# Performance work log

Measured on AMD Instinct MI355X. Metric: run time of the kernel, lower is better.

The kernel has to match this reference:

```python
import jax, jax.numpy as jnp
import numpy as np

SIZE_MIN, SIZE_MAX = 10.0, 40.0
CROP = 28


def convert_to_box_list(x):
    # [B, C, W, H] -> [W*H, B, C]
    b, c, w, h = x.shape
    return jnp.transpose(x, (2, 3, 0, 1)).reshape(w * h, b, c)


def invert_convert_to_box_list(x, w, h):
    # [W*H, B, C] -> [B, C, W, H]
    n, b, c = x.shape
    return jnp.transpose(x.reshape(w, h, b, c), (2, 3, 0, 1))


def bilinear_sample(img, x, y):
    # img: [C, W, H]; x, y: pixel coords of shape S -> [C, *S]; zero outside.
    C, W, H = img.shape
    x0 = jnp.floor(x); y0 = jnp.floor(y)
    x1 = x0 + 1.0; y1 = y0 + 1.0
    wx1 = x - x0; wx0 = 1.0 - wx1
    wy1 = y - y0; wy0 = 1.0 - wy1
    def fetch(xi, yi):
        valid = ((xi >= 0) & (xi < W) & (yi >= 0) & (yi < H)).astype(img.dtype)
        xc = jnp.clip(xi, 0, W - 1).astype(jnp.int32)
        yc = jnp.clip(yi, 0, H - 1).astype(jnp.int32)
        return img[:, xc, yc] * valid
    return (fetch(x0, y0) * (wx0 * wy0) + fetch(x1, y0) * (wx1 * wy0)
            + fetch(x0, y1) * (wx0 * wy1) + fetch(x1, y1) * (wx1 * wy1))


def crop(bx, by, bw, bh, big, ws, hs):
    # bx..bh: [k, B]; big: [B, C, W, H] -> [k, B, C, ws, hs]
    u = (jnp.arange(ws) + 0.5) / ws
    v = (jnp.arange(hs) + 0.5) / hs
    xs = bx[..., None] - 0.5 * bw[..., None] + u * bw[..., None] - 0.5  # [k,B,ws]
    ys = by[..., None] - 0.5 * bh[..., None] + v * bh[..., None] - 0.5  # [k,B,hs]
    def one(xr, yr, img):
        X = jnp.broadcast_to(xr[:, None], (ws, hs))
        Y = jnp.broadcast_to(yr[None, :], (ws, hs))
        return bilinear_sample(img, X, Y)
    return jax.vmap(jax.vmap(one, (0, 0, 0)), (0, 0, None))(xs, ys, big)


def uncrop(bx, by, bw, bh, small, Wb, Hb):
    # small: [k, B, C, ws, hs] -> [k, B, C, Wb, Hb] (zero outside each box)
    ws, hs = small.shape[-2], small.shape[-1]
    Xc = jnp.arange(Wb) + 0.5
    Yc = jnp.arange(Hb) + 0.5
    xs = (Xc - (bx[..., None] - 0.5 * bw[..., None])) / bw[..., None] * ws - 0.5
    ys = (Yc - (by[..., None] - 0.5 * bh[..., None])) / bh[..., None] * hs - 0.5
    def one(xr, yr, img):
        X = jnp.broadcast_to(xr[:, None], (Wb, Hb))
        Y = jnp.broadcast_to(yr[None, :], (Wb, Hb))
        return bilinear_sample(img, X, Y)
    return jax.vmap(jax.vmap(one, (0, 0, 0)), (0, 0, 0))(xs, ys, small)


def tmaps_to_bb(tmaps, W_raw, H_raw):
    # tmaps: [B, 4, nw, nh] in (0,1) -> box lists [n_all, B]
    nw, nh = tmaps.shape[-2], tmaps.shape[-1]
    tx, ty, tw, th = tmaps[:, 0], tmaps[:, 1], tmaps[:, 2], tmaps[:, 3]
    ix = jnp.arange(nw, dtype=tmaps.dtype)[:, None]
    iy = jnp.arange(nh, dtype=tmaps.dtype)[None, :]
    bx_map = W_raw * (ix + tx) / nw
    by_map = H_raw * (iy + ty) / nh
    bw_map = SIZE_MIN + (SIZE_MAX - SIZE_MIN) * tw
    bh_map = SIZE_MIN + (SIZE_MAX - SIZE_MIN) * th
    tolist = lambda m: convert_to_box_list(m[:, None]).squeeze(-1)
    return tolist(bx_map), tolist(by_map), tolist(bw_map), tolist(bh_map)


def forward_core(logit_mu, zwhere_mu, zwhere_std, eps_zwhere, eps_zinstance,
                 features, w_zwhere, b_zwhere, w_enc, b_enc, w_dec, b_dec, n_objects_max):
    B, Cf, W_raw, H_raw = features.shape
    nw, nh = logit_mu.shape[-2], logit_mu.shape[-1]

    # zwhere posterior sample + KL vs N(0,1)
    zwhere_sample_map = zwhere_mu + zwhere_std * eps_zwhere
    zwhere_kl_map = 0.5 * (zwhere_mu ** 2 + zwhere_std ** 2) - jnp.log(zwhere_std) - 0.5

    # decode zwhere (1x1 conv) -> sigmoid tmaps -> boxes
    tmaps = jax.nn.sigmoid(jnp.einsum('bzwh,cz->bcwh', zwhere_sample_map, w_zwhere)
                           + b_zwhere[None, :, None, None])
    bx_all, by_all, bw_all, bh_all = tmaps_to_bb(tmaps, W_raw, H_raw)

    area_all = bw_all * bh_all
    area_map = invert_convert_to_box_list(area_all[..., None], nw, nh)

    # c sample = logit map (deterministic relaxation of the DPP/Bernoulli sample)
    c_sample_map = logit_mu
    prob_map = jax.nn.sigmoid(c_sample_map)
    c_all = convert_to_box_list(c_sample_map).squeeze(-1)   # [n_all, B]
    prob_all = convert_to_box_list(prob_map).squeeze(-1)

    # top-k per batch element (indices constant wrt grads)
    k = min(n_objects_max, c_all.shape[0])
    idx = jax.lax.stop_gradient(jax.lax.top_k(c_all.T, k)[1].T)  # [k, B]
    take = lambda t: jnp.take_along_axis(t, idx, axis=0)
    c_few, prob_few = take(c_all), take(prob_all)
    bx_few, by_few, bw_few, bh_few = take(bx_all), take(by_all), take(bw_all), take(bh_all)

    zwhere_sample_all = convert_to_box_list(zwhere_sample_map)  # [n_all, B, Z]
    zwhere_kl_all = convert_to_box_list(zwhere_kl_map)
    idx_z = idx[..., None]
    zwhere_sample_few = jnp.take_along_axis(zwhere_sample_all, idx_z, axis=0)
    zwhere_kl_few = jnp.take_along_axis(zwhere_kl_all, idx_z, axis=0)

    # crop full-res features at the k boxes -> [k, B, Cf, CROP, CROP]
    cropped = crop(bx_few, by_few, bw_few, bh_few, features, CROP, CROP)

    # encoder zinstance (flatten + linear -> mu, std)
    flat = cropped.reshape(k, B, -1)
    enc = jnp.einsum('kbf,df->kbd', flat, w_enc) + b_enc
    dim_z = enc.shape[-1] // 2
    zi_mu = enc[..., :dim_z]
    zi_std = jax.nn.softplus(enc[..., dim_z:]) + 1e-4
    zi_sample = zi_mu + zi_std * eps_zinstance
    zi_kl = 0.5 * (zi_mu ** 2 + zi_std ** 2) - jnp.log(zi_std) - 0.5

    # decoder zinstance (linear -> [k, B, 2, CROP, CROP])
    dec = jnp.einsum('kbz,fz->kbf', zi_sample, w_dec) + b_dec
    raw = dec.reshape(k, B, 2, CROP, CROP)
    small = jnp.concatenate([jax.nn.softplus(raw[..., :1, :, :]),
                             jax.nn.sigmoid(raw[..., 1:, :, :])], axis=-3)

    big_stuff = uncrop(bx_few, by_few, bw_few, bh_few,
                       small * c_few[..., None, None, None], W_raw, H_raw)
    big_weight = big_stuff[..., :1, :, :]
    big_img = big_stuff[..., 1:, :, :]

    # from_weights_to_masks over box dim (dim=-5 of [k,B,1,W,H])
    sum_w = jnp.sum(big_weight, axis=0, keepdims=True)
    big_mask = jnp.tanh(sum_w) * (big_weight / jnp.maximum(sum_w, 1e-6))
    big_mask_non = jnp.tanh(big_weight)

    return (prob_map, area_map, c_few, prob_few, bx_few, by_few, bw_few, bh_few,
            big_mask, big_mask_non, big_img,
            zwhere_sample_few, zwhere_kl_few, zi_sample, zi_kl)


def setup_inputs() -> dict:
    key = jax.random.key(0)
    ks = jax.random.split(key, 9)
    B, NW, NH = 8, 32, 32
    W_RAW = H_RAW = 128
    CF, ZW, ZI, K = 32, 8, 32, 48
    fan_in = CF * CROP * CROP
    return {
        "logit_mu": jax.random.normal(ks[0], (B, 1, NW, NH), jnp.float32),
        "zwhere_mu": 0.5 * jax.random.normal(ks[1], (B, ZW, NW, NH), jnp.float32),
        "zwhere_std": jax.random.uniform(ks[2], (B, ZW, NW, NH), jnp.float32, 0.1, 1.0),
        "eps_zwhere": jax.random.normal(ks[3], (B, ZW, NW, NH), jnp.float32),
        "eps_zinstance": jax.random.normal(ks[4], (K, B, ZI), jnp.float32),
        "features": jax.random.normal(ks[5], (B, CF, W_RAW, H_RAW), jnp.float32),
        "w_zwhere": 0.3 * jax.random.normal(ks[6], (4, ZW), jnp.float32),
        "b_zwhere": jnp.zeros((4,), jnp.float32),
        "w_enc": jax.random.normal(ks[7], (2 * ZI, fan_in), jnp.float32) / np.sqrt(fan_in).astype(np.float32),
        "b_enc": jnp.zeros((2 * ZI,), jnp.float32),
        "w_dec": jax.random.normal(ks[8], (2 * CROP * CROP, ZI), jnp.float32) / np.sqrt(ZI).astype(np.float32),
        "b_dec": jnp.zeros((2 * CROP * CROP,), jnp.float32),
        "n_objects_max": 48,
    }


def reference(logit_mu, zwhere_mu, zwhere_std, eps_zwhere, eps_zinstance, features,
              w_zwhere, b_zwhere, w_enc, b_enc, w_dec, b_dec, n_objects_max):
    return forward_core(logit_mu, zwhere_mu, zwhere_std, eps_zwhere, eps_zinstance,
                        features, w_zwhere, b_zwhere, w_enc, b_enc, w_dec, b_dec,
                        n_objects_max)
```

## Files before the change

kernel.cpp:

```cpp
#include <hip/hip_runtime.h>
#include <math.h>

#define B 8
#define NWD 32
#define NHD 32
#define NBOX 1024
#define ZWD 8
#define ZID 32
#define KOBJ 48
#define CFEAT 32
#define WRAW 128
#define HRAW 128
#define CR 28
#define CR2 784
#define FAN 25088
#define KB 384

#define OFF_PROB   0
#define OFF_AREA   8192
#define OFF_CFEW   16384
#define OFF_PFEW   16768
#define OFF_BXF    17152
#define OFF_BYF    17536
#define OFF_BWF    17920
#define OFF_BHF    18304
#define OFF_BMASK  18688
#define OFF_BMASKN 6310144
#define OFF_BIMG   12601600
#define OFF_ZWS    18893056
#define OFF_ZWK    18896128
#define OFF_ZIS    18899200
#define OFF_ZIK    18911488

#define WS_SMALL 32768

#define SCR_PART 0
#define SCR_WT   2752512

#define FSPLIT 112
#define FPB 224
#define MKB 16
#define KSTR 232
#define TAPN (MKB*28)

typedef __attribute__((ext_vector_type(8))) short bfrag;
typedef __attribute__((ext_vector_type(4))) float f32x4;

__device__ __forceinline__ float sigm(float x){ return 1.0f/(1.0f+expf(-x)); }
__device__ __forceinline__ float softpl(float x){ return fmaxf(x,0.0f) + log1pf(expf(-fabsf(x))); }
__device__ __forceinline__ float ftanh(float x){
  float t = __expf(2.0f*x);
  return 1.0f - __fdividef(2.0f, t + 1.0f);
}
__device__ __forceinline__ unsigned short f2bf(float f){
  unsigned u = __float_as_uint(f);
  unsigned r = u + 0x7FFFu + ((u >> 16) & 1u);
  return (unsigned short)(r >> 16);
}
__device__ __forceinline__ unsigned okey(float f){
  unsigned b = __float_as_uint(f);
  return b ^ ((b & 0x80000000u) ? 0xFFFFFFFFu : 0x80000000u);
}

__global__ __launch_bounds__(256) void wconv_kernel(
    const float* __restrict__ wenc, unsigned short* __restrict__ wt){
  const int gid = blockIdx.x*256 + threadIdx.x;
  const int lane = gid & 63;
  const int rest = gid >> 6;
  const int t = rest & 3;
  const int rest2 = rest >> 2;
  const int s = rest2 % 7;
  const int fs = rest2 / 7;
  const int d = t*16 + (lane & 15);
  const int k0 = fs*FPB + s*32 + (lane >> 4)*8;
  const float* src = wenc + (size_t)d*FAN + k0;
  float4 a = *(const float4*)src;
  float4 b = *(const float4*)(src + 4);
  unsigned long long p0 = (unsigned long long)f2bf(a.x)
    | ((unsigned long long)f2bf(a.y) << 16)
    | ((unsigned long long)f2bf(a.z) << 32)
    | ((unsigned long long)f2bf(a.w) << 48);
  unsigned long long p1 = (unsigned long long)f2bf(b.x)
    | ((unsigned long long)f2bf(b.y) << 16)
    | ((unsigned long long)f2bf(b.z) << 32)
    | ((unsigned long long)f2bf(b.w) << 48);
  unsigned short* dst = wt + (size_t)gid*8;
  *(unsigned long long*)dst       = p0;
  *(unsigned long long*)(dst + 4) = p1;
}

__global__ __launch_bounds__(256) void maps_topk_kernel(
    const float* __restrict__ logit, const float* __restrict__ zmu,
    const float* __restrict__ zstd, const float* __restrict__ zeps,
    const float* __restrict__ wz, const float* __restrict__ bz,
    float* __restrict__ out){
  const int b  = blockIdx.x >> 2;
  const int sb = blockIdx.x & 3;
  const int tid = threadIdx.x;
  __shared__ __align__(16) unsigned su[NBOX];
  #pragma unroll
  for (int u = 0; u < 4; u++){
    int j = tid + u*256;
    su[j] = okey(logit[b*NBOX + j]);
  }
  const int n = sb*256 + tid;
  const int w = n >> 5, h = n & 31;
  float acc0=bz[0], acc1=bz[1], acc2=bz[2], acc3=bz[3];
  #pragma unroll
  for(int z=0; z<ZWD; z++){
    int id = ((b*ZWD + z)*NWD + w)*NHD + h;
    float s = zmu[id] + zstd[id]*zeps[id];
    acc0 += s*wz[0*ZWD+z]; acc1 += s*wz[1*ZWD+z];
    acc2 += s*wz[2*ZWD+z]; acc3 += s*wz[3*ZWD+z];
  }
  float tx=sigm(acc0), ty=sigm(acc1), tw=sigm(acc2), th=sigm(acc3);
  float bx = (128.0f*((float)w + tx))/32.0f;
  float by = (128.0f*((float)h + ty))/32.0f;
  float bwv = 10.0f + 30.0f*tw;
  float bhv = 10.0f + 30.0f*th;
  float lg = logit[b*NBOX + n];
  out[OFF_PROB + b*NBOX + n] = sigm(lg);
  out[OFF_AREA + b*NBOX + n] = bwv*bhv;
  __syncthreads();
  const unsigned ui = su[n];
  const uint4* su4 = (const uint4*)su;
  int rank = 0;
  #pragma unroll 4
  for (int jq = 0; jq < NBOX/4; jq++){
    uint4 v = su4[jq];
    int j = jq*4;
    rank += (v.x > ui || (v.x == ui && j   < n)) ? 1 : 0;
    rank += (v.y > ui || (v.y == ui && j+1 < n)) ? 1 : 0;
    rank += (v.z > ui || (v.z == ui && j+2 < n)) ? 1 : 0;
    rank += (v.w > ui || (v.w == ui && j+3 < n)) ? 1 : 0;
  }
  if (rank < KOBJ){
    out[OFF_CFEW + rank*B + b] = lg;
    out[OFF_PFEW + rank*B + b] = sigm(lg);
    out[OFF_BXF  + rank*B + b] = bx;
    out[OFF_BYF  + rank*B + b] = by;
    out[OFF_BWF  + rank*B + b] = bwv;
    out[OFF_BHF  + rank*B + b] = bhv;
    #pragma unroll
    for(int z=0; z<ZWD; z++){
      int id = ((b*ZWD + z)*NWD + w)*NHD + h;
      float mu = zmu[id], sd = zstd[id];
      out[OFF_ZWS + (rank*B+b)*ZWD + z] = mu + sd*zeps[id];
      out[OFF_ZWK + (rank*B+b)*ZWD + z] = 0.5f*(mu*mu + sd*sd) - logf(sd) - 0.5f;
    }
  }
}

__global__ __launch_bounds__(256, 8) void enc_kernel(
    const float* __restrict__ feat, const unsigned short* __restrict__ wt,
    const float* __restrict__ outc, float* __restrict__ part){
  __shared__ __align__(16) unsigned short cl[MKB*KSTR];
  __shared__ float2 wxs[TAPN]; __shared__ int2 xos[TAPN];
  __shared__ float2 wys[TAPN]; __shared__ int2 yos[TAPN];
  __shared__ float rAx[MKB], rSx[MKB], rAy[MKB], rSy[MKB];
  const int tid = threadIdx.x;
  const int fs  = blockIdx.x % FSPLIT;
  const int kb0 = (blockIdx.x / FSPLIT) * MKB;
  if (tid < MKB){
    float bx = outc[OFF_BXF + kb0 + tid];
    float by = outc[OFF_BYF + kb0 + tid];
    float bw = outc[OFF_BWF + kb0 + tid];
    float bh = outc[OFF_BHF + kb0 + tid];
    float sx = bw * (1.0f/(float)CR), sy = bh * (1.0f/(float)CR);
    rSx[tid] = sx; rSy[tid] = sy;
    rAx[tid] = bx - 0.5f*bw + 0.5f*sx - 0.5f;
    rAy[tid] = by - 0.5f*bh + 0.5f*sy - 0.5f;
  }
  __syncthreads();
  #pragma unroll
  for (int it = 0; it < 4; it++){
    int idx = it*256 + tid;
    if (idx < 2*TAPN){
      int isy = idx >= TAPN;
      int q = idx - (isy ? TAPN : 0);
      int rr = q / 28, i = q - rr*28;
      float A = isy ? rAy[rr] : rAx[rr];
      float S = isy ? rSy[rr] : rSx[rr];
      float x = fmaf((float)i, S, A);
      float x0f = floorf(x); int x0 = (int)x0f;
      float w1 = x - x0f, w0 = 1.0f - w1;
      if ((unsigned)x0     >= WRAW) w0 = 0.f;
      if ((unsigned)(x0+1) >= WRAW) w1 = 0.f;
      int c0 = min(max(x0,0),WRAW-1), c1 = min(max(x0+1,0),WRAW-1);
      if (isy){ wys[q] = make_float2(w0,w1); yos[q] = make_int2(c0, c1); }
      else    { wxs[q] = make_float2(w0,w1); xos[q] = make_int2(c0*HRAW, c1*HRAW); }
    }
  }
  __syncthreads();
  const int fc0 = fs*FPB;
  #pragma unroll 2
  for (int u = 0; u < 14; u++){
    int idx = u*256 + tid;
    int rr = idx / FPB, ff = idx - rr*FPB;
    int f = fc0 + ff;
    int c = f / CR2; int p = f - c*CR2;
    int i = p / CR;  int j = p - i*CR;
    const float* img = feat + (size_t)(((kb0+rr) & (B-1))*CFEAT + c)*(WRAW*HRAW);
    float2 wx = wxs[rr*28 + i]; int2 xo = xos[rr*28 + i];
    float2 wy = wys[rr*28 + j]; int2 yo = yos[rr*28 + j];
    float v = (img[xo.x+yo.x]*wy.x + img[xo.x+yo.y]*wy.y)*wx.x
            + (img[xo.y+yo.x]*wy.x + img[xo.y+yo.y]*wy.y)*wx.y;
    cl[rr*KSTR + ff] = f2bf(v);
  }
  __syncthreads();
  const int lane = tid & 63, wv = tid >> 6;
  const int lr = lane & 15, lg = lane >> 4;
  f32x4 acc = {0.f,0.f,0.f,0.f};
  const unsigned short* arow  = &cl[lr*KSTR + lg*8];
  const unsigned short* bbase = wt + (size_t)fs*14336 + wv*512 + lane*8;
  #pragma unroll
  for (int s = 0; s < 7; s++){
    bfrag a = *(const bfrag*)(arow + s*32);
    bfrag b = *(const bfrag*)(bbase + s*2048);
    acc = __builtin_amdgcn_mfma_f32_16x16x32_bf16(a, b, acc, 0, 0, 0);
  }
  float* dst = part + ((size_t)fs*KB + kb0)*64;
  #pragma unroll
  for (int r = 0; r < 4; r++){
    int row = lg*4 + r;
    dst[row*64 + wv*16 + lr] = acc[r];
  }
}

__global__ __launch_bounds__(256) void zi_dec_kernel(
    const float* __restrict__ part, const float* __restrict__ benc,
    const float* __restrict__ ieps, const float* __restrict__ wdec,
    const float* __restrict__ bdec, float* __restrict__ out,
    float* __restrict__ ws){
  int kb = blockIdx.x;
  int d = threadIdx.x & 63, seg = threadIdx.x >> 6;
  float s0=0.f, s1=0.f, s2=0.f, s3=0.f;
  for (int f = seg; f < FSPLIT; f += 16){
    s0 += part[((size_t)(f   )*KB + kb)*64 + d];
    s1 += part[((size_t)(f+ 4)*KB + kb)*64 + d];
    s2 += part[((size_t)(f+ 8)*KB + kb)*64 + d];
    s3 += part[((size_t)(f+12)*KB + kb)*64 + d];
  }
  __shared__ float red[4][64];
  __shared__ float zs[ZID];
  __shared__ float cf_s;
  red[seg][d] = (s0+s1) + (s2+s3);
  __syncthreads();
  if (threadIdx.x < ZID){
    int dd = threadIdx.x;
    float mu = benc[dd]     + red[0][dd]     + red[1][dd]     + red[2][dd]     + red[3][dd];
    float pe = benc[ZID+dd] + red[0][ZID+dd] + red[1][ZID+dd] + red[2][ZID+dd] + red[3][ZID+dd];
    float sd = softpl(pe) + 1e-4f;
    float zsv = mu + sd*ieps[kb*ZID + dd];
    out[OFF_ZIS + kb*ZID + dd] = zsv;
    out[OFF_ZIK + kb*ZID + dd] = 0.5f*(mu*mu + sd*sd) - logf(sd) - 0.5f;
    zs[dd] = zsv;
  }
  if (threadIdx.x == 0) cf_s = out[OFF_CFEW + kb];
  __syncthreads();
  float cf = cf_s;
  for (int f = threadIdx.x; f < 2*CR2; f += 256){
    float a = bdec[f];
    #pragma unroll
    for (int q = 0; q < 8; q++){
      float4 w4 = *(const float4*)&wdec[f*ZID + q*4];
      a = fmaf(zs[q*4+0], w4.x, a);
      a = fmaf(zs[q*4+1], w4.y, a);
      a = fmaf(zs[q*4+2], w4.z, a);
      a = fmaf(zs[q*4+3], w4.w, a);
    }
    float v = (f < CR2) ? softpl(a) : sigm(a);
    ws[WS_SMALL + (size_t)kb*(2*CR2) + f] = v*cf;
  }
}

__global__ __launch_bounds__(256) void uncrop_compose_kernel(
    const float* __restrict__ ws, float* __restrict__ out){
  const int t = blockIdx.x*256 + threadIdx.x;
  const int b = t >> 14, p = t & 16383;
  const int X = p >> 7, Y = p & 127;
  __shared__ float sAx[KOBJ], sSx[KOBJ], sAy[KOBJ], sSy[KOBJ];
  if (threadIdx.x < KOBJ){
    int k = threadIdx.x;
    float bx = out[OFF_BXF + k*B + b], bw = out[OFF_BWF + k*B + b];
    float by = out[OFF_BYF + k*B + b], bh = out[OFF_BHF + k*B + b];
    float ix = __fdividef((float)CR, bw), iy = __fdividef((float)CR, bh);
    sSx[k] = ix; sAx[k] = (0.5f*bw - bx)*ix - 0.5f;
    sSy[k] = iy; sAy[k] = (0.5f*bh - by)*iy - 0.5f;
  }
  __syncthreads();
  const float xc = (float)X + 0.5f, yc = (float)Y + 0.5f;
  float wr[KOBJ];
  float sum = 0.f;
  #pragma unroll
  for (int k = 0; k < KOBJ; k++){
    float x = fmaf(xc, sSx[k], sAx[k]);
    float y = fmaf(yc, sSy[k], sAy[k]);
    const float* sm = ws + WS_SMALL + (size_t)(k*B + b)*(2*CR2);
    float x0f = floorf(x), y0f = floorf(y);
    int x0 = (int)x0f, y0 = (int)y0f;
    float wx1 = x - x0f, wx0 = 1.0f - wx1;
    float wy1 = y - y0f, wy0 = 1.0f - wy1;
    if ((unsigned)x0     >= CR) wx0 = 0.f;
    if ((unsigned)(x0+1) >= CR) wx1 = 0.f;
    if ((unsigned)y0     >= CR) wy0 = 0.f;
    if ((unsigned)(y0+1) >= CR) wy1 = 0.f;
    int x0c = min(max(x0,0),CR-1), x1c = min(max(x0+1,0),CR-1);
    int y0c = min(max(y0,0),CR-1), y1c = min(max(y0+1,0),CR-1);
    const float* r0 = sm + x0c*CR;
    const float* r1 = sm + x1c*CR;
    float v0 = (r0[y0c]*wy0 + r0[y1c]*wy1)*wx0 + (r1[y0c]*wy0 + r1[y1c]*wy1)*wx1;
    const float* q0 = r0 + CR2;
    const float* q1 = r1 + CR2;
    float v1 = (q0[y0c]*wy0 + q0[y1c]*wy1)*wx0 + (q1[y0c]*wy0 + q1[y1c]*wy1)*wx1;
    wr[k] = v0; sum += v0;
    out[OFF_BIMG + (size_t)(k*B + b)*16384 + p] = v1;
  }
  float th = ftanh(sum);
  float inv = 1.0f / fmaxf(sum, 1e-6f);
  #pragma unroll
  for (int k = 0; k < KOBJ; k++){
    size_t o = (size_t)(k*B + b)*16384 + p;
    out[OFF_BMASK  + o] = th * (wr[k] * inv);
    out[OFF_BMASKN + o] = ftanh(wr[k]);
  }
}

extern "C" void kernel_launch(void* const* d_in, const int* in_sizes, int n_in,
                              void* d_out, int out_size, void* d_ws, size_t ws_size,
                              hipStream_t stream) {
  (void)in_sizes; (void)n_in; (void)out_size; (void)ws_size;
  const float* logit = (const float*)d_in[0];
  const float* zmu   = (const float*)d_in[1];
  const float* zstd  = (const float*)d_in[2];
  const float* zeps  = (const float*)d_in[3];
  const float* ieps  = (const float*)d_in[4];
  const float* feat  = (const float*)d_in[5];
  const float* wz    = (const float*)d_in[6];
  const float* bz    = (const float*)d_in[7];
  const float* wenc  = (const float*)d_in[8];
  const float* benc  = (const float*)d_in[9];
  const float* wdec  = (const float*)d_in[10];
  const float* bdec  = (const float*)d_in[11];
  float* out = (float*)d_out;
  float* ws  = (float*)d_ws;
  float* scr = out + OFF_BMASK;
  float* part = scr + SCR_PART;
  unsigned short* wt = (unsigned short*)(scr + SCR_WT);

  wconv_kernel        <<<(FAN*64)/(256*8), 256, 0, stream>>>(wenc, wt);
  maps_topk_kernel    <<<B*4, 256, 0, stream>>>(logit, zmu, zstd, zeps, wz, bz, out);
  enc_kernel          <<<(KB/MKB)*FSPLIT, 256, 0, stream>>>(feat, wt, out, part);
  zi_dec_kernel       <<<KB, 256, 0, stream>>>(part, benc, ieps, wdec, bdec, out, ws);
  uncrop_compose_kernel<<<(B*WRAW*HRAW)/256, 256, 0, stream>>>(ws, out);
}
```

Measured before the change: 95.50 us.

## Fuse prep kernels and double-buffer encoder sampling across feature chunks

Merges the weight-conversion and top-k map kernels into one launch. The encoder kernel now handles four feature chunks per block, cutting the split factor from 112 to 28, and double-buffers the sampled crop tile in shared memory so bilinear gathers for the next chunk overlap the MFMA on the current one. Fewer partial sums leave a smaller reduction in zi_dec. The trade-off is fewer encoder blocks, which lowers parallelism, and more shared memory per block, which may reduce occupancy.

```diff
diff --git a/kernel.cpp b/kernel.cpp
--- a/kernel.cpp
+++ b/kernel.cpp
@@ -37,8 +37,10 @@
 #define SCR_PART 0
 #define SCR_WT   2752512
 
-#define FSPLIT 112
-#define FPB 224
+#define FSPLIT 28
+#define FPB 896
+#define CHK 224
+#define NCH 4
 #define MKB 16
 #define KSTR 232
 #define TAPN (MKB*28)
@@ -62,42 +64,43 @@
   return b ^ ((b & 0x80000000u) ? 0xFFFFFFFFu : 0x80000000u);
 }
 
-__global__ __launch_bounds__(256) void wconv_kernel(
-    const float* __restrict__ wenc, unsigned short* __restrict__ wt){
-  const int gid = blockIdx.x*256 + threadIdx.x;
-  const int lane = gid & 63;
-  const int rest = gid >> 6;
-  const int t = rest & 3;
-  const int rest2 = rest >> 2;
-  const int s = rest2 % 7;
-  const int fs = rest2 / 7;
-  const int d = t*16 + (lane & 15);
-  const int k0 = fs*FPB + s*32 + (lane >> 4)*8;
-  const float* src = wenc + (size_t)d*FAN + k0;
-  float4 a = *(const float4*)src;
-  float4 b = *(const float4*)(src + 4);
-  unsigned long long p0 = (unsigned long long)f2bf(a.x)
-    | ((unsigned long long)f2bf(a.y) << 16)
-    | ((unsigned long long)f2bf(a.z) << 32)
-    | ((unsigned long long)f2bf(a.w) << 48);
-  unsigned long long p1 = (unsigned long long)f2bf(b.x)
-    | ((unsigned long long)f2bf(b.y) << 16)
-    | ((unsigned long long)f2bf(b.z) << 32)
-    | ((unsigned long long)f2bf(b.w) << 48);
-  unsigned short* dst = wt + (size_t)gid*8;
-  *(unsigned long long*)dst       = p0;
-  *(unsigned long long*)(dst + 4) = p1;
-}
-
-__global__ __launch_bounds__(256) void maps_topk_kernel(
+__global__ __launch_bounds__(256) void prep_kernel(
+    const float* __restrict__ wenc, unsigned short* __restrict__ wt,
     const float* __restrict__ logit, const float* __restrict__ zmu,
     const float* __restrict__ zstd, const float* __restrict__ zeps,
     const float* __restrict__ wz, const float* __restrict__ bz,
     float* __restrict__ out){
-  const int b  = blockIdx.x >> 2;
-  const int sb = blockIdx.x & 3;
+  __shared__ __align__(16) unsigned su[NBOX];
+  if (blockIdx.x < 784){
+    const int gid = blockIdx.x*256 + threadIdx.x;
+    const int lane = gid & 63;
+    const int rest = gid >> 6;
+    const int t = rest & 3;
+    const int rest2 = rest >> 2;
+    const int s = rest2 % 7;
+    const int fsc = rest2 / 7;
+    const int d = t*16 + (lane & 15);
+    const int k0 = fsc*CHK + s*32 + (lane >> 4)*8;
+    const float* src = wenc + (size_t)d*FAN + k0;
+    float4 a = *(const float4*)src;
+    float4 b = *(const float4*)(src + 4);
+    unsigned long long p0 = (unsigned long long)f2bf(a.x)
+      | ((unsigned long long)f2bf(a.y) << 16)
+      | ((unsigned long long)f2bf(a.z) << 32)
+      | ((unsigned long long)f2bf(a.w) << 48);
+    unsigned long long p1 = (unsigned long long)f2bf(b.x)
+      | ((unsigned long long)f2bf(b.y) << 16)
+      | ((unsigned long long)f2bf(b.z) << 32)
+      | ((unsigned long long)f2bf(b.w) << 48);
+    unsigned short* dst = wt + (size_t)gid*8;
+    *(unsigned long long*)dst       = p0;
+    *(unsigned long long*)(dst + 4) = p1;
+    return;
+  }
+  const int bid = blockIdx.x - 784;
+  const int b  = bid >> 2;
+  const int sb = bid & 3;
   const int tid = threadIdx.x;
-  __shared__ __align__(16) unsigned su[NBOX];
   #pragma unroll
   for (int u = 0; u < 4; u++){
     int j = tid + u*256;
@@ -151,10 +154,32 @@
   }
 }
 
+__device__ __forceinline__ void sample_chunk(
+    int tid, int fs, int ch, int kb0, const float* __restrict__ feat,
+    const float2* wxs, const int2* xos, const float2* wys, const int2* yos,
+    unsigned short* cl){
+  const int kc0 = fs*FPB + ch*CHK;
+  #pragma unroll 2
+  for (int u = 0; u < 14; u++){
+    int idx = u*256 + tid;
+    int rr = idx / CHK, ff = idx - rr*CHK;
+    int f = kc0 + ff;
+    int c = f / CR2; int p = f - c*CR2;
+    int i = p / CR;  int j = p - i*CR;
+    const float* img = feat + (size_t)(((kb0+rr) & (B-1))*CFEAT + c)*(WRAW*HRAW);
+    float2 wx = wxs[rr*28 + i]; int2 xo = xos[rr*28 + i];
+    float2 wy = wys[rr*28 + j]; int2 yo = yos[rr*28 + j];
+    float v = (img[xo.x+yo.x]*wy.x + img[xo.x+yo.y]*wy.y)*wx.x
+            + (img[xo.y+yo.x]*wy.x + img[xo.y+yo.y]*wy.y)*wx.y;
+    cl[rr*KSTR + ff] = f2bf(v);
+  }
+}
+
 __global__ __launch_bounds__(256, 8) void enc_kernel(
     const float* __restrict__ feat, const unsigned short* __restrict__ wt,
     const float* __restrict__ outc, float* __restrict__ part){
-  __shared__ __align__(16) unsigned short cl[MKB*KSTR];
+  __shared__ __align__(16) unsigned short cl0[MKB*KSTR];
+  __shared__ __align__(16) unsigned short cl1[MKB*KSTR];
   __shared__ float2 wxs[TAPN]; __shared__ int2 xos[TAPN];
   __shared__ float2 wys[TAPN]; __shared__ int2 yos[TAPN];
   __shared__ float rAx[MKB], rSx[MKB], rAy[MKB], rSy[MKB];
@@ -192,32 +217,26 @@
     }
   }
   __syncthreads();
-  const int fc0 = fs*FPB;
-  #pragma unroll 2
-  for (int u = 0; u < 14; u++){
-    int idx = u*256 + tid;
-    int rr = idx / FPB, ff = idx - rr*FPB;
-    int f = fc0 + ff;
-    int c = f / CR2; int p = f - c*CR2;
-    int i = p / CR;  int j = p - i*CR;
-    const float* img = feat + (size_t)(((kb0+rr) & (B-1))*CFEAT + c)*(WRAW*HRAW);
-    float2 wx = wxs[rr*28 + i]; int2 xo = xos[rr*28 + i];
-    float2 wy = wys[rr*28 + j]; int2 yo = yos[rr*28 + j];
-    float v = (img[xo.x+yo.x]*wy.x + img[xo.x+yo.y]*wy.y)*wx.x
-            + (img[xo.y+yo.x]*wy.x + img[xo.y+yo.y]*wy.y)*wx.y;
-    cl[rr*KSTR + ff] = f2bf(v);
-  }
-  __syncthreads();
   const int lane = tid & 63, wv = tid >> 6;
   const int lr = lane & 15, lg = lane >> 4;
   f32x4 acc = {0.f,0.f,0.f,0.f};
-  const unsigned short* arow  = &cl[lr*KSTR + lg*8];
-  const unsigned short* bbase = wt + (size_t)fs*14336 + wv*512 + lane*8;
-  #pragma unroll
-  for (int s = 0; s < 7; s++){
-    bfrag a = *(const bfrag*)(arow + s*32);
-    bfrag b = *(const bfrag*)(bbase + s*2048);
-    acc = __builtin_amdgcn_mfma_f32_16x16x32_bf16(a, b, acc, 0, 0, 0);
+  sample_chunk(tid, fs, 0, kb0, feat, wxs, xos, wys, yos, cl0);
+  __syncthreads();
+  #pragma unroll
+  for (int ch = 0; ch < NCH; ch++){
+    unsigned short* cur = (ch & 1) ? cl1 : cl0;
+    unsigned short* nxt = (ch & 1) ? cl0 : cl1;
+    if (ch < NCH-1)
+      sample_chunk(tid, fs, ch+1, kb0, feat, wxs, xos, wys, yos, nxt);
+    const unsigned short* arow  = &cur[lr*KSTR + lg*8];
+    const unsigned short* bbase = wt + (size_t)(fs*NCH + ch)*14336 + wv*512 + lane*8;
+    #pragma unroll
+    for (int s = 0; s < 7; s++){
+      bfrag a = *(const bfrag*)(arow + s*32);
+      bfrag b = *(const bfrag*)(bbase + s*2048);
+      acc = __builtin_amdgcn_mfma_f32_16x16x32_bf16(a, b, acc, 0, 0, 0);
+    }
+    __syncthreads();
   }
   float* dst = part + ((size_t)fs*KB + kb0)*64;
   #pragma unroll
@@ -234,17 +253,15 @@
     float* __restrict__ ws){
   int kb = blockIdx.x;
   int d = threadIdx.x & 63, seg = threadIdx.x >> 6;
-  float s0=0.f, s1=0.f, s2=0.f, s3=0.f;
-  for (int f = seg; f < FSPLIT; f += 16){
-    s0 += part[((size_t)(f   )*KB + kb)*64 + d];
-    s1 += part[((size_t)(f+ 4)*KB + kb)*64 + d];
-    s2 += part[((size_t)(f+ 8)*KB + kb)*64 + d];
-    s3 += part[((size_t)(f+12)*KB + kb)*64 + d];
-  }
+  float s0=0.f, s1=0.f;
+  for (int f = seg; f < FSPLIT; f += 8)
+    s0 += part[((size_t)f*KB + kb)*64 + d];
+  for (int f = seg+4; f < FSPLIT; f += 8)
+    s1 += part[((size_t)f*KB + kb)*64 + d];
   __shared__ float red[4][64];
   __shared__ float zs[ZID];
   __shared__ float cf_s;
-  red[seg][d] = (s0+s1) + (s2+s3);
+  red[seg][d] = s0 + s1;
   __syncthreads();
   if (threadIdx.x < ZID){
     int dd = threadIdx.x;
@@ -348,8 +365,7 @@
   float* part = scr + SCR_PART;
   unsigned short* wt = (unsigned short*)(scr + SCR_WT);
 
-  wconv_kernel        <<<(FAN*64)/(256*8), 256, 0, stream>>>(wenc, wt);
-  maps_topk_kernel    <<<B*4, 256, 0, stream>>>(logit, zmu, zstd, zeps, wz, bz, out);
+  prep_kernel         <<<784 + B*4, 256, 0, stream>>>(wenc, wt, logit, zmu, zstd, zeps, wz, bz, out);
   enc_kernel          <<<(KB/MKB)*FSPLIT, 256, 0, stream>>>(feat, wt, out, part);
   zi_dec_kernel       <<<KB, 256, 0, stream>>>(part, benc, ieps, wdec, bdec, out, ws);
   uncrop_compose_kernel<<<(B*WRAW*HRAW)/256, 256, 0, stream>>>(ws, out);
```

Result: no change. 95.10 us (-0.4%).
